# Kernel optimization log

Hardware: AMD Instinct MI355X
Metric: run time of the kernel (lower is better)

Reference implementation:

```python
import jax, jax.numpy as jnp
import numpy as np

D_MODEL = 1024
N_HEADS = 16
NEG_INF = -1e9


def setup_inputs() -> dict:
    key = jax.random.key(0)
    ks = jax.random.split(key, 12)
    B, S, D = 2, 2048, D_MODEL
    Q = jax.random.normal(ks[0], (B, S, D), jnp.float32)
    K = jax.random.normal(ks[1], (B, S, D), jnp.float32)
    V = jax.random.normal(ks[2], (B, S, D), jnp.float32)
    # causal mask (1 = attend, 0 = masked), per mask==0 -> -1e9 in the source
    mask = jnp.tril(jnp.ones((S, S), bool))[None, :, :].repeat(B, axis=0)
    sc = 1.0 / np.sqrt(D)
    Wq = jax.random.normal(ks[3], (D, D), jnp.float32) * sc
    bq = jnp.zeros((D,), jnp.float32)
    Wk = jax.random.normal(ks[4], (D, D), jnp.float32) * sc
    bk = jnp.zeros((D,), jnp.float32)
    Wv = jax.random.normal(ks[5], (D, D), jnp.float32) * sc
    bv = jnp.zeros((D,), jnp.float32)
    Wo = jax.random.normal(ks[6], (D, D), jnp.float32) * sc
    bo = jnp.zeros((D,), jnp.float32)
    return {"Q": Q, "K": K, "V": V, "mask": mask,
            "Wq": Wq, "bq": bq, "Wk": Wk, "bk": bk,
            "Wv": Wv, "bv": bv, "Wo": Wo, "bo": bo}


def reference(Q, K, V, mask, Wq, bq, Wk, bk, Wv, bv, Wo, bo):
    B, S, D = Q.shape
    H = N_HEADS
    dk = D // H
    scale = jnp.asarray(dk, Q.dtype) ** -0.5
    # projections (torch nn.Linear: x @ W^T + b), split heads -> [B,H,S,dk]
    q = (Q @ Wq.T + bq).reshape(B, S, H, dk).transpose(0, 2, 1, 3)
    k = (K @ Wk.T + bk).reshape(B, S, H, dk).transpose(0, 2, 1, 3)
    v = (V @ Wv.T + bv).reshape(B, S, H, dk).transpose(0, 2, 1, 3)
    scores = jnp.einsum('bhqd,bhkd->bhqk', q, k) * scale  # [B,H,S,S]
    scores = jnp.where(mask[:, None, :, :], scores, NEG_INF)
    attn = jax.nn.softmax(scores, axis=-1)
    # dropout is identity in eval mode
    out = jnp.einsum('bhqk,bhkd->bhqd', attn, v)
    out = out.transpose(0, 2, 1, 3).reshape(B, S, D)
    return out @ Wo.T + bo, attn
```

## Files before the change

kernel.cpp:

```cpp
#include <hip/hip_runtime.h>
#include <cstddef>
#include <cstdint>

typedef unsigned short u16;
typedef unsigned int   u32;
typedef __attribute__((ext_vector_type(8))) short          bf16x8;
typedef __attribute__((ext_vector_type(4))) float          f32x4;
typedef __attribute__((ext_vector_type(4))) unsigned short u16x4;
typedef __attribute__((ext_vector_type(4))) unsigned int   u32x4;

#define S_LEN 2048
#define DM    1024
#define BHD   32
#define NROWS 4096
#define QSCALE 0.18033688011112042f
#define SOFTC  28.853900817779268f

__device__ __forceinline__ u16 f2bf(float x) {
  u32 u = __float_as_uint(x);
  return (u16)((u + 0x7fffu + ((u >> 16) & 1u)) >> 16);
}
__device__ __forceinline__ float bf2f(u16 h) {
  return __uint_as_float(((u32)h) << 16);
}
__device__ __forceinline__ void gld16(const void* g, void* l) {
  __builtin_amdgcn_global_load_lds((const __attribute__((address_space(1))) void*)g,
                                   (__attribute__((address_space(3))) void*)l, 16, 0, 0);
}
#define MFMA16(a, b, c) __builtin_amdgcn_mfma_f32_16x16x32_bf16(a, b, c, 0, 0, 0)

__global__ __launch_bounds__(256) void splitk(const float* __restrict__ src,
                                              u16* __restrict__ hi,
                                              u16* __restrict__ lo, int n4) {
  for (int i = blockIdx.x * 256 + threadIdx.x; i < n4; i += gridDim.x * 256) {
    float4 v = ((const float4*)src)[i];
    u16x4 h, l;
    {
      u16 a = f2bf(v.x); h[0] = a; l[0] = f2bf(v.x - bf2f(a));
      a = f2bf(v.y); h[1] = a; l[1] = f2bf(v.y - bf2f(a));
      a = f2bf(v.z); h[2] = a; l[2] = f2bf(v.z - bf2f(a));
      a = f2bf(v.w); h[3] = a; l[3] = f2bf(v.w - bf2f(a));
    }
    *(u16x4*)&hi[(size_t)i * 4] = h;
    *(u16x4*)&lo[(size_t)i * 4] = l;
  }
}

template<int EPI>
__global__ __launch_bounds__(256) void gemm_split(
    const u16* __restrict__ Ah, const u16* __restrict__ Al,
    const u16* __restrict__ Bh, const u16* __restrict__ Bl,
    const float* __restrict__ bias,
    u16* __restrict__ Oh, u16* __restrict__ Ol, float* __restrict__ Of,
    float scale)
{
  __shared__ __align__(16) u16 lds[2][12288];
  const int t = threadIdx.x;
  const int lane = t & 63, w = t >> 6;
  const int u = lane >> 4, c15 = lane & 15;
  const int wm = w >> 1, wn = w & 1;
  const int bm = blockIdx.x * 128, bn = blockIdx.y * 64;

  f32x4 acc[4][2];
#pragma unroll
  for (int i = 0; i < 4; ++i)
#pragma unroll
    for (int j = 0; j < 2; ++j) acc[i][j] = (f32x4){0.f, 0.f, 0.f, 0.f};

  auto stage = [&](int buf, int kb) {
    const int x = t >> 2, p = t & 3;
    const int co = kb + 8 * (p ^ ((x >> 1) & 3));
    u16* L = lds[buf];
    gld16(Ah + (size_t)(bm + x) * DM + co,      L + t * 8);
    gld16(Ah + (size_t)(bm + 64 + x) * DM + co, L + 2048 + t * 8);
    gld16(Al + (size_t)(bm + x) * DM + co,      L + 4096 + t * 8);
    gld16(Al + (size_t)(bm + 64 + x) * DM + co, L + 6144 + t * 8);
    gld16(Bh + (size_t)(bn + x) * DM + co,      L + 8192 + t * 8);
    gld16(Bl + (size_t)(bn + x) * DM + co,      L + 10240 + t * 8);
  };

  stage(0, 0);
  __syncthreads();
  int buf = 0;
  for (int kb = 0; kb < DM; kb += 32) {
    if (kb + 32 < DM) stage(buf ^ 1, kb + 32);
    const u16* L = lds[buf];
    bf16x8 a_h[4], a_l[4], b_h[2], b_l[2];
#pragma unroll
    for (int i = 0; i < 4; ++i) {
      const int r = wm * 64 + 16 * i + c15;
      const int off = r * 32 + 8 * (u ^ ((r >> 1) & 3));
      a_h[i] = *(const bf16x8*)&L[off];
      a_l[i] = *(const bf16x8*)&L[4096 + off];
    }
#pragma unroll
    for (int j = 0; j < 2; ++j) {
      const int n = wn * 32 + 16 * j + c15;
      const int off = n * 32 + 8 * (u ^ ((n >> 1) & 3));
      b_h[j] = *(const bf16x8*)&L[8192 + off];
      b_l[j] = *(const bf16x8*)&L[10240 + off];
    }
#pragma unroll
    for (int i = 0; i < 4; ++i)
#pragma unroll
      for (int j = 0; j < 2; ++j) {
        acc[i][j] = MFMA16(a_h[i], b_h[j], acc[i][j]);
        acc[i][j] = MFMA16(a_h[i], b_l[j], acc[i][j]);
        acc[i][j] = MFMA16(a_l[i], b_h[j], acc[i][j]);
      }
    __syncthreads();
    buf ^= 1;
  }

#pragma unroll
  for (int j = 0; j < 2; ++j) {
    const int n = bn + wn * 32 + 16 * j + c15;
    const float bv = bias[n];
#pragma unroll
    for (int i = 0; i < 4; ++i) {
      float v[4];
#pragma unroll
      for (int r = 0; r < 4; ++r) v[r] = (acc[i][j][r] + bv) * scale;
      const int m0 = bm + wm * 64 + 16 * i + 4 * u;
      if (EPI == 2) {
#pragma unroll
        for (int r = 0; r < 4; ++r) Of[(size_t)(m0 + r) * DM + n] = v[r];
      } else if (EPI == 0) {
#pragma unroll
        for (int r = 0; r < 4; ++r) {
          const int m = m0 + r;
          const int b_ = m >> 11, s_ = m & 2047, h_ = n >> 6, d_ = n & 63;
          const size_t idx = (((size_t)(b_ * 16 + h_)) * S_LEN + s_) * 64 + d_;
          u16 hh = f2bf(v[r]);
          Oh[idx] = hh; Ol[idx] = f2bf(v[r] - bf2f(hh));
        }
      } else {
        u16x4 hv, lv;
#pragma unroll
        for (int r = 0; r < 4; ++r) {
          u16 hh = f2bf(v[r]); hv[r] = hh; lv[r] = f2bf(v[r] - bf2f(hh));
        }
        const int b_ = m0 >> 11, s_ = m0 & 2047, h_ = n >> 6, d_ = n & 63;
        const size_t idx = (((size_t)(b_ * 16 + h_)) * 64 + d_) * S_LEN + s_;
        *(u16x4*)&Oh[idx] = hv; *(u16x4*)&Ol[idx] = lv;
      }
    }
  }
}

__global__ __launch_bounds__(256) void attn_mfma(
    const u16* __restrict__ Qh, const u16* __restrict__ Ql,
    const u16* __restrict__ Kh, const u16* __restrict__ Kl,
    const u16* __restrict__ Vh, const u16* __restrict__ Vl,
    float* __restrict__ attnO, u16* __restrict__ Oh, u16* __restrict__ Ol)
{
  __shared__ __align__(16) u16 Kbuf[2][2][4096];
  __shared__ __align__(16) u16 Vbuf[2][4096];
  __shared__ __align__(16) u32 Pbuf[4096];

  const int t = threadIdx.x;
  const int bh = blockIdx.x;
  const int pair = blockIdx.y;
  const int lane = t & 63, w = t >> 6;
  const int u = lane >> 4, c15 = lane & 15;
  const size_t kvbase = (size_t)bh * S_LEN * 64;

  auto stageK = [&](int bb, int tk) {
    const int x = t >> 3, p = t & 7;
    const int co = 8 * (p ^ (x & 7));
    const u16* bH = Kh + kvbase + (size_t)tk * 4096;
    const u16* bL = Kl + kvbase + (size_t)tk * 4096;
    gld16(bH + (size_t)x * 64 + co,        &Kbuf[bb][0][t * 8]);
    gld16(bH + (size_t)(x + 32) * 64 + co, &Kbuf[bb][0][2048 + t * 8]);
    gld16(bL + (size_t)x * 64 + co,        &Kbuf[bb][1][t * 8]);
    gld16(bL + (size_t)(x + 32) * 64 + co, &Kbuf[bb][1][2048 + t * 8]);
  };
  auto stageV = [&](int tk) {
    const int x = t >> 3, p = t & 7;
    const int co = 8 * (p ^ (x & 7));
    const u16* bH = Vh + kvbase + (size_t)tk * 64;
    const u16* bL = Vl + kvbase + (size_t)tk * 64;
    gld16(bH + (size_t)x * S_LEN + co,        &Vbuf[0][t * 8]);
    gld16(bH + (size_t)(x + 32) * S_LEN + co, &Vbuf[0][2048 + t * 8]);
    gld16(bL + (size_t)x * S_LEN + co,        &Vbuf[1][t * 8]);
    gld16(bL + (size_t)(x + 32) * S_LEN + co, &Vbuf[1][2048 + t * 8]);
  };

  {
    const int r = t >> 2, cq = t & 3;
    const float4 z = make_float4(0.f, 0.f, 0.f, 0.f);
#pragma unroll
    for (int which = 0; which < 2; ++which) {
      const int qb = which ? (31 - pair) : pair;
      float4* rowp = (float4*)(attnO + ((size_t)bh * S_LEN + qb * 64 + r) * S_LEN);
      for (int c4 = (qb + 1) * 16 + cq; c4 < 512; c4 += 4) rowp[c4] = z;
    }
  }

  for (int which = 0; which < 2; ++which) {
    const int qb = which ? (31 - pair) : pair;
    const int q0 = qb * 64;

    const size_t qrow = kvbase + (size_t)(q0 + 16 * w + c15) * 64;
    bf16x8 qfh[2], qfl[2];
    qfh[0] = *(const bf16x8*)&Qh[qrow + 8 * u];
    qfh[1] = *(const bf16x8*)&Qh[qrow + 32 + 8 * u];
    qfl[0] = *(const bf16x8*)&Ql[qrow + 8 * u];
    qfl[1] = *(const bf16x8*)&Ql[qrow + 32 + 8 * u];

    float lsum[4] = {0.f, 0.f, 0.f, 0.f};

    int b = 0;
    stageK(0, 0);
    __syncthreads();
    for (int tk = 0; tk <= qb; ++tk) {
      if (tk < qb) stageK(b ^ 1, tk + 1);
      f32x4 sacc[4];
#pragma unroll
      for (int j = 0; j < 4; ++j) sacc[j] = (f32x4){0.f, 0.f, 0.f, 0.f};
#pragma unroll
      for (int j = 0; j < 4; ++j) {
        const int srow = 16 * j + c15;
#pragma unroll
        for (int h = 0; h < 2; ++h) {
          const int off = srow * 64 + 8 * ((4 * h + u) ^ (srow & 7));
          bf16x8 kbh = *(const bf16x8*)&Kbuf[b][0][off];
          bf16x8 kbl = *(const bf16x8*)&Kbuf[b][1][off];
          sacc[j] = MFMA16(qfh[h], kbh, sacc[j]);
          sacc[j] = MFMA16(qfh[h], kbl, sacc[j]);
          sacc[j] = MFMA16(qfl[h], kbh, sacc[j]);
        }
      }
      const bool dg = (tk == qb);
#pragma unroll
      for (int r = 0; r < 4; ++r) {
        const int qg = 16 * w + 4 * u + r;
        float part = 0.f;
#pragma unroll
        for (int j = 0; j < 4; ++j) {
          const int sg = tk * 64 + 16 * j + c15;
          const bool keep = (!dg) || (sg <= q0 + qg);
          part += keep ? exp2f(sacc[j][r] - SOFTC) : 0.f;
        }
        part += __shfl_xor(part, 1);
        part += __shfl_xor(part, 2);
        part += __shfl_xor(part, 4);
        part += __shfl_xor(part, 8);
        lsum[r] += part;
      }
      __syncthreads();
      b ^= 1;
    }

    float linv[4];
#pragma unroll
    for (int r = 0; r < 4; ++r) linv[r] = 1.0f / lsum[r];

    b = 0;
    stageK(0, 0);
    __syncthreads();
    f32x4 oacc[4];
#pragma unroll
    for (int j = 0; j < 4; ++j) oacc[j] = (f32x4){0.f, 0.f, 0.f, 0.f};

    for (int tk = 0; tk <= qb; ++tk) {
      stageV(tk);
      if (tk < qb) stageK(b ^ 1, tk + 1);
      f32x4 sacc[4];
#pragma unroll
      for (int j = 0; j < 4; ++j) sacc[j] = (f32x4){0.f, 0.f, 0.f, 0.f};
#pragma unroll
      for (int j = 0; j < 4; ++j) {
        const int srow = 16 * j + c15;
#pragma unroll
        for (int h = 0; h < 2; ++h) {
          const int off = srow * 64 + 8 * ((4 * h + u) ^ (srow & 7));
          bf16x8 kbh = *(const bf16x8*)&Kbuf[b][0][off];
          bf16x8 kbl = *(const bf16x8*)&Kbuf[b][1][off];
          sacc[j] = MFMA16(qfh[h], kbh, sacc[j]);
          sacc[j] = MFMA16(qfh[h], kbl, sacc[j]);
          sacc[j] = MFMA16(qfl[h], kbh, sacc[j]);
        }
      }
      const bool dg = (tk == qb);
#pragma unroll
      for (int r = 0; r < 4; ++r) {
        const int qg = 16 * w + 4 * u + r;
        const float iv = linv[r];
#pragma unroll
        for (int j = 0; j < 4; ++j) {
          const int sl = 16 * j + c15;
          const int sg = tk * 64 + sl;
          const bool keep = (!dg) || (sg <= q0 + qg);
          const float pn = keep ? exp2f(sacc[j][r] - SOFTC) * iv : 0.f;
          attnO[((size_t)bh * S_LEN + q0 + qg) * S_LEN + sg] = pn;
          const u16 ph = f2bf(pn);
          const u16 pl = f2bf(pn - bf2f(ph));
          Pbuf[qg * 64 + (((sl >> 2) ^ (qg & 15)) << 2) + (sl & 3)] =
              (u32)ph | ((u32)pl << 16);
        }
      }
      __syncthreads();
      {
        const int qloc = 16 * w + c15;
#pragma unroll
        for (int h = 0; h < 2; ++h) {
          u32x4 p0 = *(const u32x4*)&Pbuf[qloc * 64 + (((8 * h + 2 * u + 0) ^ (qloc & 15)) << 2)];
          u32x4 p1 = *(const u32x4*)&Pbuf[qloc * 64 + (((8 * h + 2 * u + 1) ^ (qloc & 15)) << 2)];
          union { bf16x8 v; u32 x[4]; } H, L;
          H.x[0] = (p0[0] & 0xffffu) | (p0[1] << 16);
          H.x[1] = (p0[2] & 0xffffu) | (p0[3] << 16);
          H.x[2] = (p1[0] & 0xffffu) | (p1[1] << 16);
          H.x[3] = (p1[2] & 0xffffu) | (p1[3] << 16);
          L.x[0] = (p0[0] >> 16) | (p0[1] & 0xffff0000u);
          L.x[1] = (p0[2] >> 16) | (p0[3] & 0xffff0000u);
          L.x[2] = (p1[0] >> 16) | (p1[1] & 0xffff0000u);
          L.x[3] = (p1[2] >> 16) | (p1[3] & 0xffff0000u);
#pragma unroll
          for (int j = 0; j < 4; ++j) {
            const int dr = 16 * j + c15;
            const int off = dr * 64 + 8 * ((4 * h + u) ^ (dr & 7));
            bf16x8 vH = *(const bf16x8*)&Vbuf[0][off];
            bf16x8 vL = *(const bf16x8*)&Vbuf[1][off];
            oacc[j] = MFMA16(H.v, vH, oacc[j]);
            oacc[j] = MFMA16(H.v, vL, oacc[j]);
            oacc[j] = MFMA16(L.v, vH, oacc[j]);
          }
        }
      }
      __syncthreads();
      b ^= 1;
    }

    const int bb = bh >> 4, hh = bh & 15;
#pragma unroll
    for (int j = 0; j < 4; ++j) {
      const int d = 16 * j + c15;
#pragma unroll
      for (int r = 0; r < 4; ++r) {
        const int qg = q0 + 16 * w + 4 * u + r;
        const float v = oacc[j][r];
        const u16 hi = f2bf(v);
        const size_t idx = ((size_t)bb * S_LEN + qg) * DM + hh * 64 + d;
        Oh[idx] = hi; Ol[idx] = f2bf(v - bf2f(hi));
      }
    }
  }
}

extern "C" void kernel_launch(void* const* d_in, const int* in_sizes, int n_in,
                              void* d_out, int out_size, void* d_ws, size_t ws_size,
                              hipStream_t stream) {
  const float* Q  = (const float*)d_in[0];
  const float* K  = (const float*)d_in[1];
  const float* V  = (const float*)d_in[2];
  const float* Wq = (const float*)d_in[4];
  const float* bq = (const float*)d_in[5];
  const float* Wk = (const float*)d_in[6];
  const float* bk = (const float*)d_in[7];
  const float* Wv = (const float*)d_in[8];
  const float* bv = (const float*)d_in[9];
  const float* Wo = (const float*)d_in[10];
  const float* bo = (const float*)d_in[11];

  float* out  = (float*)d_out;
  float* attn = out + (size_t)NROWS * DM;

  u16* base = (u16*)d_ws;
  const size_t XN = (size_t)NROWS * DM;
  const size_t WN = (size_t)DM * DM;
  u16* xh  = base;            u16* xl  = xh  + XN;
  u16* wh  = xl  + XN;        u16* wl  = wh  + WN;
  u16* Qph = wl  + WN;        u16* Qpl = Qph + XN;
  u16* Kph = Qpl + XN;        u16* Kpl = Kph + XN;
  u16* Vth = Kpl + XN;        u16* Vtl = Vth + XN;
  u16* Oh2 = Vtl + XN;        u16* Ol2 = Oh2 + XN;

  const dim3 cgrid(1024), cb(256);
  const dim3 ggrid(NROWS / 128, DM / 64), gb(256);
  const dim3 agrid(BHD, 16), ab(256);

  splitk<<<cgrid, cb, 0, stream>>>(Q,  xh, xl, (int)(XN / 4));
  splitk<<<cgrid, cb, 0, stream>>>(Wq, wh, wl, (int)(WN / 4));
  gemm_split<0><<<ggrid, gb, 0, stream>>>(xh, xl, wh, wl, bq, Qph, Qpl, nullptr, QSCALE);
  splitk<<<cgrid, cb, 0, stream>>>(K,  xh, xl, (int)(XN / 4));
  splitk<<<cgrid, cb, 0, stream>>>(Wk, wh, wl, (int)(WN / 4));
  gemm_split<0><<<ggrid, gb, 0, stream>>>(xh, xl, wh, wl, bk, Kph, Kpl, nullptr, 1.0f);
  splitk<<<cgrid, cb, 0, stream>>>(V,  xh, xl, (int)(XN / 4));
  splitk<<<cgrid, cb, 0, stream>>>(Wv, wh, wl, (int)(WN / 4));
  gemm_split<1><<<ggrid, gb, 0, stream>>>(xh, xl, wh, wl, bv, Vth, Vtl, nullptr, 1.0f);
  attn_mfma<<<agrid, ab, 0, stream>>>(Qph, Qpl, Kph, Kpl, Vth, Vtl, attn, Oh2, Ol2);
  splitk<<<cgrid, cb, 0, stream>>>(Wo, wh, wl, (int)(WN / 4));
  gemm_split<2><<<ggrid, gb, 0, stream>>>(Oh2, Ol2, wh, wl, bo, nullptr, nullptr, out, 1.0f);
}
```

Measured before the change: 882.2 us.

## Batch splits into one launch, enlarge GEMM tiles, restructure attention P staging

Merges the seven split-to-bf16 conversions into a single launch with per-input pointers, which needs more workspace. GEMM blocks grow to 128x128 with a 1D grid swizzle, improving operand reuse but lowering the block count. The attention kernel stages fp32 probabilities in padded LDS, converts them with packed bf16 instructions, and writes the attention matrix with coalesced float4 stores. It also defers the row-sum shuffle reduction to the end, adds setprio around MFMA sections, and remaps blocks to spread heads across the grid.

```diff
diff --git a/kernel.cpp b/kernel.cpp
--- a/kernel.cpp
+++ b/kernel.cpp
@@ -7,11 +7,9 @@
 typedef __attribute__((ext_vector_type(8))) short          bf16x8;
 typedef __attribute__((ext_vector_type(4))) float          f32x4;
 typedef __attribute__((ext_vector_type(4))) unsigned short u16x4;
-typedef __attribute__((ext_vector_type(4))) unsigned int   u32x4;
 
 #define S_LEN 2048
 #define DM    1024
-#define BHD   32
 #define NROWS 4096
 #define QSCALE 0.18033688011112042f
 #define SOFTC  28.853900817779268f
@@ -20,29 +18,34 @@
   u32 u = __float_as_uint(x);
   return (u16)((u + 0x7fffu + ((u >> 16) & 1u)) >> 16);
 }
-__device__ __forceinline__ float bf2f(u16 h) {
-  return __uint_as_float(((u32)h) << 16);
+__device__ __forceinline__ float bf2f(u16 h) { return __uint_as_float(((u32)h) << 16); }
+__device__ __forceinline__ u32 cvtpk(float lo, float hi) {
+  u32 r; asm("v_cvt_pk_bf16_f32 %0, %1, %2" : "=v"(r) : "v"(lo), "v"(hi)); return r;
 }
 __device__ __forceinline__ void gld16(const void* g, void* l) {
   __builtin_amdgcn_global_load_lds((const __attribute__((address_space(1))) void*)g,
                                    (__attribute__((address_space(3))) void*)l, 16, 0, 0);
 }
-#define MFMA16(a, b, c) __builtin_amdgcn_mfma_f32_16x16x32_bf16(a, b, c, 0, 0, 0)
-
-__global__ __launch_bounds__(256) void splitk(const float* __restrict__ src,
-                                              u16* __restrict__ hi,
-                                              u16* __restrict__ lo, int n4) {
-  for (int i = blockIdx.x * 256 + threadIdx.x; i < n4; i += gridDim.x * 256) {
-    float4 v = ((const float4*)src)[i];
-    u16x4 h, l;
-    {
-      u16 a = f2bf(v.x); h[0] = a; l[0] = f2bf(v.x - bf2f(a));
-      a = f2bf(v.y); h[1] = a; l[1] = f2bf(v.y - bf2f(a));
-      a = f2bf(v.z); h[2] = a; l[2] = f2bf(v.z - bf2f(a));
-      a = f2bf(v.w); h[3] = a; l[3] = f2bf(v.w - bf2f(a));
-    }
-    *(u16x4*)&hi[(size_t)i * 4] = h;
-    *(u16x4*)&lo[(size_t)i * 4] = l;
+__device__ __forceinline__ int swz4(int r) { return (r & 3) ^ ((r >> 2) & 3); }
+#define MFMA16(a,b,c) __builtin_amdgcn_mfma_f32_16x16x32_bf16(a,b,c,0,0,0)
+
+struct SplitArgs { const float* s[7]; u16* h[7]; u16* l[7]; int n4[7]; };
+
+__global__ __launch_bounds__(256) void splitk7(SplitArgs a) {
+  const int y = blockIdx.y;
+  const float* s = a.s[y];
+  u16* h = a.h[y]; u16* l = a.l[y];
+  const int n4 = a.n4[y];
+  const int step = gridDim.x * 256;
+  for (int i = blockIdx.x * 256 + threadIdx.x; i < n4; i += step) {
+    float4 v = ((const float4*)s)[i];
+    u16x4 hh, ll; u16 x;
+    x = f2bf(v.x); hh[0] = x; ll[0] = f2bf(v.x - bf2f(x));
+    x = f2bf(v.y); hh[1] = x; ll[1] = f2bf(v.y - bf2f(x));
+    x = f2bf(v.z); hh[2] = x; ll[2] = f2bf(v.z - bf2f(x));
+    x = f2bf(v.w); hh[3] = x; ll[3] = f2bf(v.w - bf2f(x));
+    *(u16x4*)&h[(size_t)i * 4] = hh;
+    *(u16x4*)&l[(size_t)i * 4] = ll;
   }
 }
 
@@ -54,29 +57,34 @@
     u16* __restrict__ Oh, u16* __restrict__ Ol, float* __restrict__ Of,
     float scale)
 {
-  __shared__ __align__(16) u16 lds[2][12288];
+  __shared__ __align__(16) u16 lds[2][16384];
   const int t = threadIdx.x;
+  const int id = blockIdx.x;
+  const int bn = (id & 7) * 128;
+  const int bm = (id >> 3) * 128;
   const int lane = t & 63, w = t >> 6;
   const int u = lane >> 4, c15 = lane & 15;
-  const int wm = w >> 1, wn = w & 1;
-  const int bm = blockIdx.x * 128, bn = blockIdx.y * 64;
-
-  f32x4 acc[4][2];
+  const int wr = (w >> 1) * 64, wc = (w & 1) * 64;
+
+  f32x4 acc[4][4];
 #pragma unroll
   for (int i = 0; i < 4; ++i)
 #pragma unroll
-    for (int j = 0; j < 2; ++j) acc[i][j] = (f32x4){0.f, 0.f, 0.f, 0.f};
+    for (int j = 0; j < 4; ++j) acc[i][j] = (f32x4){0.f, 0.f, 0.f, 0.f};
 
   auto stage = [&](int buf, int kb) {
-    const int x = t >> 2, p = t & 3;
-    const int co = kb + 8 * (p ^ ((x >> 1) & 3));
     u16* L = lds[buf];
-    gld16(Ah + (size_t)(bm + x) * DM + co,      L + t * 8);
-    gld16(Ah + (size_t)(bm + 64 + x) * DM + co, L + 2048 + t * 8);
-    gld16(Al + (size_t)(bm + x) * DM + co,      L + 4096 + t * 8);
-    gld16(Al + (size_t)(bm + 64 + x) * DM + co, L + 6144 + t * 8);
-    gld16(Bh + (size_t)(bn + x) * DM + co,      L + 8192 + t * 8);
-    gld16(Bl + (size_t)(bn + x) * DM + co,      L + 10240 + t * 8);
+#pragma unroll
+    for (int pp = 0; pp < 2; ++pp) {
+      const int q = t + pp * 256;
+      const int row = q >> 2;
+      const int ch = (q & 3) ^ swz4(row);
+      const int co = kb + 8 * ch;
+      gld16(Ah + (size_t)(bm + row) * DM + co, L + q * 8);
+      gld16(Al + (size_t)(bm + row) * DM + co, L + 4096 + q * 8);
+      gld16(Bh + (size_t)(bn + row) * DM + co, L + 8192 + q * 8);
+      gld16(Bl + (size_t)(bn + row) * DM + co, L + 12288 + q * 8);
+    }
   };
 
   stage(0, 0);
@@ -85,43 +93,41 @@
   for (int kb = 0; kb < DM; kb += 32) {
     if (kb + 32 < DM) stage(buf ^ 1, kb + 32);
     const u16* L = lds[buf];
-    bf16x8 a_h[4], a_l[4], b_h[2], b_l[2];
+    bf16x8 ah[4], al[4];
 #pragma unroll
     for (int i = 0; i < 4; ++i) {
-      const int r = wm * 64 + 16 * i + c15;
-      const int off = r * 32 + 8 * (u ^ ((r >> 1) & 3));
-      a_h[i] = *(const bf16x8*)&L[off];
-      a_l[i] = *(const bf16x8*)&L[4096 + off];
-    }
-#pragma unroll
-    for (int j = 0; j < 2; ++j) {
-      const int n = wn * 32 + 16 * j + c15;
-      const int off = n * 32 + 8 * (u ^ ((n >> 1) & 3));
-      b_h[j] = *(const bf16x8*)&L[8192 + off];
-      b_l[j] = *(const bf16x8*)&L[10240 + off];
-    }
-#pragma unroll
-    for (int i = 0; i < 4; ++i)
-#pragma unroll
-      for (int j = 0; j < 2; ++j) {
-        acc[i][j] = MFMA16(a_h[i], b_h[j], acc[i][j]);
-        acc[i][j] = MFMA16(a_h[i], b_l[j], acc[i][j]);
-        acc[i][j] = MFMA16(a_l[i], b_h[j], acc[i][j]);
-      }
+      const int r = wr + 16 * i + c15;
+      const int off = r * 32 + 8 * (u ^ swz4(r));
+      ah[i] = *(const bf16x8*)&L[off];
+      al[i] = *(const bf16x8*)&L[4096 + off];
+    }
+#pragma unroll
+    for (int j = 0; j < 4; ++j) {
+      const int n = wc + 16 * j + c15;
+      const int off = n * 32 + 8 * (u ^ swz4(n));
+      bf16x8 bh8 = *(const bf16x8*)&L[8192 + off];
+      bf16x8 bl8 = *(const bf16x8*)&L[12288 + off];
+#pragma unroll
+      for (int i = 0; i < 4; ++i) {
+        acc[i][j] = MFMA16(ah[i], bh8, acc[i][j]);
+        acc[i][j] = MFMA16(ah[i], bl8, acc[i][j]);
+        acc[i][j] = MFMA16(al[i], bh8, acc[i][j]);
+      }
+    }
     __syncthreads();
     buf ^= 1;
   }
 
 #pragma unroll
-  for (int j = 0; j < 2; ++j) {
-    const int n = bn + wn * 32 + 16 * j + c15;
+  for (int j = 0; j < 4; ++j) {
+    const int n = bn + wc + 16 * j + c15;
     const float bv = bias[n];
 #pragma unroll
     for (int i = 0; i < 4; ++i) {
       float v[4];
 #pragma unroll
       for (int r = 0; r < 4; ++r) v[r] = (acc[i][j][r] + bv) * scale;
-      const int m0 = bm + wm * 64 + 16 * i + 4 * u;
+      const int m0 = bm + wr + 16 * i + 4 * u;
       if (EPI == 2) {
 #pragma unroll
         for (int r = 0; r < 4; ++r) Of[(size_t)(m0 + r) * DM + n] = v[r];
@@ -156,11 +162,12 @@
 {
   __shared__ __align__(16) u16 Kbuf[2][2][4096];
   __shared__ __align__(16) u16 Vbuf[2][4096];
-  __shared__ __align__(16) u32 Pbuf[4096];
+  __shared__ __align__(16) float Pbuf[64][68];
 
   const int t = threadIdx.x;
-  const int bh = blockIdx.x;
-  const int pair = blockIdx.y;
+  const int id = blockIdx.x;
+  const int bh = (id & 7) * 4 + ((id >> 3) >> 4);
+  const int pair = (id >> 3) & 15;
   const int lane = t & 63, w = t >> 6;
   const int u = lane >> 4, c15 = lane & 15;
   const size_t kvbase = (size_t)bh * S_LEN * 64;
@@ -187,13 +194,17 @@
   };
 
   {
-    const int r = t >> 2, cq = t & 3;
+    const int rr0 = t >> 4, cq = t & 15;
     const float4 z = make_float4(0.f, 0.f, 0.f, 0.f);
 #pragma unroll
     for (int which = 0; which < 2; ++which) {
-      const int qb = which ? (31 - pair) : pair;
-      float4* rowp = (float4*)(attnO + ((size_t)bh * S_LEN + qb * 64 + r) * S_LEN);
-      for (int c4 = (qb + 1) * 16 + cq; c4 < 512; c4 += 4) rowp[c4] = z;
+      const int qb2 = which ? (31 - pair) : pair;
+#pragma unroll
+      for (int pp = 0; pp < 4; ++pp) {
+        const int row = pp * 16 + rr0;
+        float4* rowp = (float4*)(attnO + ((size_t)bh * S_LEN + qb2 * 64 + row) * S_LEN);
+        for (int c4 = (qb2 + 1) * 16 + cq; c4 < 512; c4 += 16) rowp[c4] = z;
+      }
     }
   }
 
@@ -218,6 +229,7 @@
       f32x4 sacc[4];
 #pragma unroll
       for (int j = 0; j < 4; ++j) sacc[j] = (f32x4){0.f, 0.f, 0.f, 0.f};
+      __builtin_amdgcn_s_setprio(1);
 #pragma unroll
       for (int j = 0; j < 4; ++j) {
         const int srow = 16 * j + c15;
@@ -231,22 +243,17 @@
           sacc[j] = MFMA16(qfl[h], kbh, sacc[j]);
         }
       }
+      __builtin_amdgcn_s_setprio(0);
       const bool dg = (tk == qb);
 #pragma unroll
       for (int r = 0; r < 4; ++r) {
         const int qg = 16 * w + 4 * u + r;
-        float part = 0.f;
 #pragma unroll
         for (int j = 0; j < 4; ++j) {
           const int sg = tk * 64 + 16 * j + c15;
           const bool keep = (!dg) || (sg <= q0 + qg);
-          part += keep ? exp2f(sacc[j][r] - SOFTC) : 0.f;
-        }
-        part += __shfl_xor(part, 1);
-        part += __shfl_xor(part, 2);
-        part += __shfl_xor(part, 4);
-        part += __shfl_xor(part, 8);
-        lsum[r] += part;
+          lsum[r] += keep ? exp2f(sacc[j][r] - SOFTC) : 0.f;
+        }
       }
       __syncthreads();
       b ^= 1;
@@ -254,7 +261,12 @@
 
     float linv[4];
 #pragma unroll
-    for (int r = 0; r < 4; ++r) linv[r] = 1.0f / lsum[r];
+    for (int r = 0; r < 4; ++r) {
+      float s = lsum[r];
+      s += __shfl_xor(s, 1); s += __shfl_xor(s, 2);
+      s += __shfl_xor(s, 4); s += __shfl_xor(s, 8);
+      linv[r] = 1.0f / s;
+    }
 
     b = 0;
     stageK(0, 0);
@@ -269,6 +281,7 @@
       f32x4 sacc[4];
 #pragma unroll
       for (int j = 0; j < 4; ++j) sacc[j] = (f32x4){0.f, 0.f, 0.f, 0.f};
+      __builtin_amdgcn_s_setprio(1);
 #pragma unroll
       for (int j = 0; j < 4; ++j) {
         const int srow = 16 * j + c15;
@@ -282,6 +295,7 @@
           sacc[j] = MFMA16(qfl[h], kbh, sacc[j]);
         }
       }
+      __builtin_amdgcn_s_setprio(0);
       const bool dg = (tk == qb);
 #pragma unroll
       for (int r = 0; r < 4; ++r) {
@@ -292,30 +306,36 @@
           const int sl = 16 * j + c15;
           const int sg = tk * 64 + sl;
           const bool keep = (!dg) || (sg <= q0 + qg);
-          const float pn = keep ? exp2f(sacc[j][r] - SOFTC) * iv : 0.f;
-          attnO[((size_t)bh * S_LEN + q0 + qg) * S_LEN + sg] = pn;
-          const u16 ph = f2bf(pn);
-          const u16 pl = f2bf(pn - bf2f(ph));
-          Pbuf[qg * 64 + (((sl >> 2) ^ (qg & 15)) << 2) + (sl & 3)] =
-              (u32)ph | ((u32)pl << 16);
+          Pbuf[qg][sl] = keep ? exp2f(sacc[j][r] - SOFTC) * iv : 0.f;
         }
       }
       __syncthreads();
+
+      __builtin_amdgcn_s_setprio(1);
       {
         const int qloc = 16 * w + c15;
 #pragma unroll
         for (int h = 0; h < 2; ++h) {
-          u32x4 p0 = *(const u32x4*)&Pbuf[qloc * 64 + (((8 * h + 2 * u + 0) ^ (qloc & 15)) << 2)];
-          u32x4 p1 = *(const u32x4*)&Pbuf[qloc * 64 + (((8 * h + 2 * u + 1) ^ (qloc & 15)) << 2)];
+          f32x4 pa = *(const f32x4*)&Pbuf[qloc][32 * h + 8 * u];
+          f32x4 pb = *(const f32x4*)&Pbuf[qloc][32 * h + 8 * u + 4];
           union { bf16x8 v; u32 x[4]; } H, L;
-          H.x[0] = (p0[0] & 0xffffu) | (p0[1] << 16);
-          H.x[1] = (p0[2] & 0xffffu) | (p0[3] << 16);
-          H.x[2] = (p1[0] & 0xffffu) | (p1[1] << 16);
-          H.x[3] = (p1[2] & 0xffffu) | (p1[3] << 16);
-          L.x[0] = (p0[0] >> 16) | (p0[1] & 0xffff0000u);
-          L.x[1] = (p0[2] >> 16) | (p0[3] & 0xffff0000u);
-          L.x[2] = (p1[0] >> 16) | (p1[1] & 0xffff0000u);
-          L.x[3] = (p1[2] >> 16) | (p1[3] & 0xffff0000u);
+          H.x[0] = cvtpk(pa[0], pa[1]);
+          H.x[1] = cvtpk(pa[2], pa[3]);
+          H.x[2] = cvtpk(pb[0], pb[1]);
+          H.x[3] = cvtpk(pb[2], pb[3]);
+          float l0, l1;
+          l0 = pa[0] - __uint_as_float(H.x[0] << 16);
+          l1 = pa[1] - __uint_as_float(H.x[0] & 0xffff0000u);
+          L.x[0] = cvtpk(l0, l1);
+          l0 = pa[2] - __uint_as_float(H.x[1] << 16);
+          l1 = pa[3] - __uint_as_float(H.x[1] & 0xffff0000u);
+          L.x[1] = cvtpk(l0, l1);
+          l0 = pb[0] - __uint_as_float(H.x[2] << 16);
+          l1 = pb[1] - __uint_as_float(H.x[2] & 0xffff0000u);
+          L.x[2] = cvtpk(l0, l1);
+          l0 = pb[2] - __uint_as_float(H.x[3] << 16);
+          l1 = pb[3] - __uint_as_float(H.x[3] & 0xffff0000u);
+          L.x[3] = cvtpk(l0, l1);
 #pragma unroll
           for (int j = 0; j < 4; ++j) {
             const int dr = 16 * j + c15;
@@ -326,6 +346,20 @@
             oacc[j] = MFMA16(H.v, vL, oacc[j]);
             oacc[j] = MFMA16(L.v, vH, oacc[j]);
           }
+        }
+      }
+      __builtin_amdgcn_s_setprio(0);
+
+      {
+        const int rr0 = t >> 4;
+        const int cc = (t & 15) * 4;
+        float* abase = attnO + ((size_t)bh * S_LEN + q0) * S_LEN + (size_t)tk * 64;
+#pragma unroll
+        for (int pp = 0; pp < 4; ++pp) {
+          const int row = pp * 16 + rr0;
+          f32x4 pv = *(const f32x4*)&Pbuf[row][cc];
+          *(float4*)(abase + (size_t)row * S_LEN + cc) =
+              make_float4(pv[0], pv[1], pv[2], pv[3]);
         }
       }
       __syncthreads();
@@ -369,27 +403,34 @@
   u16* base = (u16*)d_ws;
   const size_t XN = (size_t)NROWS * DM;
   const size_t WN = (size_t)DM * DM;
-  u16* xh  = base;            u16* xl  = xh  + XN;
-  u16* wh  = xl  + XN;        u16* wl  = wh  + WN;
-  u16* Qph = wl  + WN;        u16* Qpl = Qph + XN;
-  u16* Kph = Qpl + XN;        u16* Kpl = Kph + XN;
-  u16* Vth = Kpl + XN;        u16* Vtl = Vth + XN;
-  u16* Oh2 = Vtl + XN;        u16* Ol2 = Oh2 + XN;
-
-  const dim3 cgrid(1024), cb(256);
-  const dim3 ggrid(NROWS / 128, DM / 64), gb(256);
-  const dim3 agrid(BHD, 16), ab(256);
-
-  splitk<<<cgrid, cb, 0, stream>>>(Q,  xh, xl, (int)(XN / 4));
-  splitk<<<cgrid, cb, 0, stream>>>(Wq, wh, wl, (int)(WN / 4));
-  gemm_split<0><<<ggrid, gb, 0, stream>>>(xh, xl, wh, wl, bq, Qph, Qpl, nullptr, QSCALE);
-  splitk<<<cgrid, cb, 0, stream>>>(K,  xh, xl, (int)(XN / 4));
-  splitk<<<cgrid, cb, 0, stream>>>(Wk, wh, wl, (int)(WN / 4));
-  gemm_split<0><<<ggrid, gb, 0, stream>>>(xh, xl, wh, wl, bk, Kph, Kpl, nullptr, 1.0f);
-  splitk<<<cgrid, cb, 0, stream>>>(V,  xh, xl, (int)(XN / 4));
-  splitk<<<cgrid, cb, 0, stream>>>(Wv, wh, wl, (int)(WN / 4));
-  gemm_split<1><<<ggrid, gb, 0, stream>>>(xh, xl, wh, wl, bv, Vth, Vtl, nullptr, 1.0f);
-  attn_mfma<<<agrid, ab, 0, stream>>>(Qph, Qpl, Kph, Kpl, Vth, Vtl, attn, Oh2, Ol2);
-  splitk<<<cgrid, cb, 0, stream>>>(Wo, wh, wl, (int)(WN / 4));
-  gemm_split<2><<<ggrid, gb, 0, stream>>>(Oh2, Ol2, wh, wl, bo, nullptr, nullptr, out, 1.0f);
-}
+  u16* xqh = base;       u16* xql = xqh + XN;
+  u16* xkh = xql + XN;   u16* xkl = xkh + XN;
+  u16* xvh = xkl + XN;   u16* xvl = xvh + XN;
+  u16* wqh = xvl + XN;   u16* wql = wqh + WN;
+  u16* wkh = wql + WN;   u16* wkl = wkh + WN;
+  u16* wvh = wkl + WN;   u16* wvl = wvh + WN;
+  u16* woh = wvl + WN;   u16* wol = woh + WN;
+  u16* Qph = wol + WN;   u16* Qpl = Qph + XN;
+  u16* Kph = Qpl + XN;   u16* Kpl = Kph + XN;
+  u16* Vth = Kpl + XN;   u16* Vtl = Vth + XN;
+  u16* Oh2 = Vtl + XN;   u16* Ol2 = Oh2 + XN;
+
+  SplitArgs sa;
+  sa.s[0] = Q;  sa.h[0] = xqh; sa.l[0] = xql; sa.n4[0] = (int)(XN / 4);
+  sa.s[1] = K;  sa.h[1] = xkh; sa.l[1] = xkl; sa.n4[1] = (int)(XN / 4);
+  sa.s[2] = V;  sa.h[2] = xvh; sa.l[2] = xvl; sa.n4[2] = (int)(XN / 4);
+  sa.s[3] = Wq; sa.h[3] = wqh; sa.l[3] = wql; sa.n4[3] = (int)(WN / 4);
+  sa.s[4] = Wk; sa.h[4] = wkh; sa.l[4] = wkl; sa.n4[4] = (int)(WN / 4);
+  sa.s[5] = Wv; sa.h[5] = wvh; sa.l[5] = wvl; sa.n4[5] = (int)(WN / 4);
+  sa.s[6] = Wo; sa.h[6] = woh; sa.l[6] = wol; sa.n4[6] = (int)(WN / 4);
+
+  splitk7<<<dim3(1024, 7), 256, 0, stream>>>(sa);
+
+  gemm_split<0><<<256, 256, 0, stream>>>(xqh, xql, wqh, wql, bq, Qph, Qpl, nullptr, QSCALE);
+  gemm_split<0><<<256, 256, 0, stream>>>(xkh, xkl, wkh, wkl, bk, Kph, Kpl, nullptr, 1.0f);
+  gemm_split<1><<<256, 256, 0, stream>>>(xvh, xvl, wvh, wvl, bv, Vth, Vtl, nullptr, 1.0f);
+
+  attn_mfma<<<512, 256, 0, stream>>>(Qph, Qpl, Kph, Kpl, Vth, Vtl, attn, Oh2, Ol2);
+
+  gemm_split<2><<<256, 256, 0, stream>>>(Oh2, Ol2, woh, wol, bo, nullptr, nullptr, out, 1.0f);
+}
```

Measured after the change: 883.9 us. About the same (+0.2%).
